# Kernel tuning notes

Measured on AMD Instinct MI355X. Metric: run time of the kernel, lower is better.

## Reference

```python
import jax, jax.numpy as jnp
import numpy as np

N, E, F_IN, H, L, G, C = 50000, 640000, 128, 128, 3, 256, 10
NEG_SLOPE = 0.2  # PyG GATConv default leaky_relu slope


def setup_inputs() -> dict:
    key = jax.random.key(0)
    ks = jax.random.split(key, 10)
    x = jax.random.normal(ks[0], (N, F_IN), jnp.float32)
    edge_index = jax.random.randint(ks[1], (2, E), 0, N, dtype=jnp.int32)
    # sorted graph ids covering all G graphs (global_max_pool segments)
    batch = (jnp.arange(N, dtype=jnp.int32) * G) // N
    s = 1.0 / np.sqrt(H)
    # 3 GAT layers all map 128->128 (F_IN == H), so stack their params
    Wc = jax.random.normal(ks[2], (L, F_IN, H), jnp.float32) * s
    a_src = jax.random.normal(ks[3], (L, H), jnp.float32) * s
    a_dst = jax.random.normal(ks[4], (L, H), jnp.float32) * s
    bc = jnp.zeros((L, H), jnp.float32)
    W1 = jax.random.normal(ks[5], (H, H), jnp.float32) * s
    b1 = jnp.zeros((H,), jnp.float32)
    W2 = jax.random.normal(ks[6], (H, C), jnp.float32) * s
    b2 = jnp.zeros((C,), jnp.float32)
    return dict(x=x, edge_index=edge_index, batch=batch, Wc=Wc, a_src=a_src,
                a_dst=a_dst, bc=bc, W1=W1, b1=b1, W2=W2, b2=b2)


def _gat_layer(h_in, W, a_s, a_d, b, src, dst):
    h = h_in @ W                                   # [N, H]
    e_s = (h * a_s).sum(-1)                        # [N] source term
    e_d = (h * a_d).sum(-1)                        # [N] target term
    e = jax.nn.leaky_relu(e_s[src] + e_d[dst], NEG_SLOPE)  # [E']
    # softmax over incoming edges of each target node
    m = jax.ops.segment_max(e, dst, num_segments=N)
    w = jnp.exp(e - m[dst])
    z = jax.ops.segment_sum(w, dst, num_segments=N)
    alpha = w / (z[dst] + 1e-16)
    out = jax.ops.segment_sum(alpha[:, None] * h[src], dst, num_segments=N)
    return out + b


def reference(x, edge_index, batch, Wc, a_src, a_dst, bc, W1, b1, W2, b2):
    loops = jnp.arange(N, dtype=edge_index.dtype)  # GATConv adds self-loops
    src = jnp.concatenate([edge_index[0], loops])
    dst = jnp.concatenate([edge_index[1], loops])
    h = x
    for l in range(L):
        h = jax.nn.relu(_gat_layer(h, Wc[l], a_src[l], a_dst[l], bc[l], src, dst))
    g = jax.ops.segment_max(h, batch, num_segments=G)  # global_max_pool [G, H]
    g = jax.nn.relu(g @ W1 + b1)
    logits = g @ W2 + b2
    return jax.nn.log_softmax(logits, axis=-1)
```

## Files before the change

### kernel.cpp

```cpp
#include <hip/hip_runtime.h>
#include <hip/hip_fp16.h>
#include <math.h>

#define N_ 50000
#define E_ 640000
#define H_ 128
#define L_ 3
#define G_ 256
#define C_ 10
#define NEG_SLOPE 0.2f

#define ABLK ((N_ + 3) / 4)
#define MAXDEG 64
#define FILL_BLKS 625
#define GEMM_BLKS ((N_ + 63) / 64)

typedef _Float16 half8 __attribute__((ext_vector_type(8)));
typedef float f32x4 __attribute__((ext_vector_type(4)));

__device__ __forceinline__ float leaky(float x) { return x > 0.f ? x : NEG_SLOPE * x; }
__device__ __forceinline__ int pi_out(int p) { return ((p & 7) << 4) + (p >> 3); }

__device__ __forceinline__ void prep_layer(int l, const float* __restrict__ Wc,
                                           const float* __restrict__ a_src,
                                           const float* __restrict__ a_dst,
                                           const float* __restrict__ bc,
                                           __half* __restrict__ Wt,
                                           float* __restrict__ bcp) {
    const float* W = Wc + l * 16384;
    __half* T = Wt + (size_t)l * 144 * 128;
    int t = threadIdx.x;
    for (int e = t; e < 16384; e += 256) {
        int n = e >> 7, p = e & 127;
        int ks = (l == 0) ? p : pi_out(p);
        T[n * 128 + p] = __float2half(W[ks * 128 + n]);
    }
    if (t < 128) {
        int p = t;
        int ks = (l == 0) ? p : pi_out(p);
        const float* as = a_src + l * 128;
        const float* ad = a_dst + l * 128;
        float s = 0.f, d = 0.f;
#pragma unroll 8
        for (int n = 0; n < 128; n++) {
            float w = W[ks * 128 + n];
            s += w * as[n];
            d += w * ad[n];
        }
        T[128 * 128 + p] = __float2half(s);
        T[129 * 128 + p] = __float2half(d);
        bcp[l * 128 + p] = bc[l * 128 + pi_out(p)];
    } else {
        int kk = t - 128;
        for (int r = 130; r < 144; r++) T[r * 128 + kk] = __float2half(0.f);
    }
}

__global__ __launch_bounds__(256) void zero_prep0(int* __restrict__ cur,
                                                  const float* __restrict__ Wc,
                                                  const float* __restrict__ a_src,
                                                  const float* __restrict__ a_dst,
                                                  const float* __restrict__ bc,
                                                  __half* __restrict__ Wt,
                                                  float* __restrict__ bcp) {
    if (blockIdx.x == 0) {
        prep_layer(0, Wc, a_src, a_dst, bc, Wt, bcp);
    } else {
        int i = (blockIdx.x - 1) * 256 + threadIdx.x;
        if (i < N_) cur[i] = 0;
    }
}

template <bool FP16IN>
__device__ __forceinline__ void gemm_body(int bid, const void* __restrict__ Av,
                                          const __half* __restrict__ Wt,
                                          __half* __restrict__ h16,
                                          float* __restrict__ es,
                                          float* __restrict__ ed,
                                          __half* __restrict__ Asw,
                                          __half* __restrict__ Bsw) {
    int tid = threadIdx.x;
    int brow = bid * 64;

    {
        int r = tid >> 2;
        int q = tid & 3;
        int grow = brow + r;
        if (FP16IN) {
            const __half* Ah = (const __half*)Av;
            float4 vv[4];
            if (grow < N_) {
                const float4* p = (const float4*)(Ah + (size_t)grow * 128 + q * 32);
#pragma unroll
                for (int s = 0; s < 4; s++) vv[s] = p[s];
            } else {
                float4 zz = make_float4(0.f, 0.f, 0.f, 0.f);
#pragma unroll
                for (int s = 0; s < 4; s++) vv[s] = zz;
            }
#pragma unroll
            for (int s = 0; s < 4; s++) {
                int kbyte = q * 64 + s * 16;
                int addr = r * 256 + (kbyte ^ ((r & 7) << 4));
                *(float4*)((char*)Asw + addr) = vv[s];
            }
        } else {
            const float* A = (const float*)Av;
            int kc = q * 32;
            float v[32];
            if (grow < N_) {
                const float4* p = (const float4*)(A + (size_t)grow * 128 + kc);
#pragma unroll
                for (int s = 0; s < 8; s++) {
                    float4 f = p[s];
                    v[s * 4] = f.x; v[s * 4 + 1] = f.y; v[s * 4 + 2] = f.z; v[s * 4 + 3] = f.w;
                }
            } else {
#pragma unroll
                for (int s = 0; s < 32; s++) v[s] = 0.f;
            }
#pragma unroll
            for (int s = 0; s < 4; s++) {
                half8 h;
#pragma unroll
                for (int j = 0; j < 8; j++) h[j] = (_Float16)v[s * 8 + j];
                int kbyte = kc * 2 + s * 16;
                int addr = r * 256 + (kbyte ^ ((r & 7) << 4));
                *(half8*)((char*)Asw + addr) = h;
            }
        }
    }
    {
        const float4* src = (const float4*)Wt;
#pragma unroll
        for (int i = 0; i < 9; i++) {
            int c = tid + i * 256;
            int o = c * 16;
            int n = o >> 8;
            float4 val = src[c];
            int addr = n * 256 + ((o & 255) ^ ((n & 7) << 4));
            *(float4*)((char*)Bsw + addr) = val;
        }
    }
    __syncthreads();

    int w = tid >> 6, l = tid & 63;
    int lrow = l & 15, lk = l >> 4;
    f32x4 acc[9];
#pragma unroll
    for (int t = 0; t < 9; t++) acc[t] = (f32x4)0.f;
#pragma unroll
    for (int kk = 0; kk < 4; kk++) {
        int kbyte = kk * 64 + lk * 16;
        int arow = w * 16 + lrow;
        half8 af = *(const half8*)((const char*)Asw + arow * 256 + (kbyte ^ ((arow & 7) << 4)));
#pragma unroll
        for (int t = 0; t < 9; t++) {
            int n = t * 16 + lrow;
            half8 bf = *(const half8*)((const char*)Bsw + n * 256 + (kbyte ^ ((n & 7) << 4)));
            acc[t] = __builtin_amdgcn_mfma_f32_16x16x32_f16(af, bf, acc[t], 0, 0, 0);
        }
    }

    int row0 = brow + w * 16 + lk * 4;
#pragma unroll
    for (int r = 0; r < 4; r++) {
        int grow = row0 + r;
        if (grow < N_) {
            half8 hv;
#pragma unroll
            for (int t = 0; t < 8; t++) hv[t] = (_Float16)acc[t][r];
            *(half8*)(h16 + (size_t)grow * 128 + lrow * 8) = hv;
            if (lrow == 0) es[grow] = acc[8][r];
            else if (lrow == 1) ed[grow] = acc[8][r];
        }
    }
}

__global__ __launch_bounds__(256) void mega0(const int* __restrict__ src,
                                             const int* __restrict__ dst,
                                             int* __restrict__ cur,
                                             int* __restrict__ col_slots,
                                             const float* __restrict__ x,
                                             const float* __restrict__ Wc,
                                             const float* __restrict__ a_src,
                                             const float* __restrict__ a_dst,
                                             const float* __restrict__ bc,
                                             __half* __restrict__ Wt,
                                             float* __restrict__ bcp,
                                             __half* __restrict__ h16,
                                             float* __restrict__ es,
                                             float* __restrict__ ed) {
    __shared__ __half Asw[64 * 128];
    __shared__ __half Bsw[144 * 128];
    int bx = blockIdx.x;
    if (bx < FILL_BLKS) {
        int b = bx * 1024 + threadIdx.x;
        int e0 = b, e1 = b + 256, e2 = b + 512, e3 = b + 768;
        int d0 = dst[e0], d1 = dst[e1], d2 = dst[e2], d3 = dst[e3];
        int s0 = src[e0], s1 = src[e1], s2 = src[e2], s3 = src[e3];
        int p0 = atomicAdd(&cur[d0], 1);
        int p1 = atomicAdd(&cur[d1], 1);
        int p2 = atomicAdd(&cur[d2], 1);
        int p3 = atomicAdd(&cur[d3], 1);
        if (p0 < MAXDEG) col_slots[d0 * MAXDEG + p0] = s0;
        if (p1 < MAXDEG) col_slots[d1 * MAXDEG + p1] = s1;
        if (p2 < MAXDEG) col_slots[d2 * MAXDEG + p2] = s2;
        if (p3 < MAXDEG) col_slots[d3 * MAXDEG + p3] = s3;
    } else if (bx < FILL_BLKS + GEMM_BLKS) {
        gemm_body<false>(bx - FILL_BLKS, x, Wt, h16, es, ed, Asw, Bsw);
    } else {
        prep_layer(bx - (FILL_BLKS + GEMM_BLKS) + 1, Wc, a_src, a_dst, bc, Wt, bcp);
    }
}

template <bool FP16IN>
__global__ __launch_bounds__(256) void gemm_mfma(const void* __restrict__ Av,
                                                 const __half* __restrict__ Wt,
                                                 __half* __restrict__ h16,
                                                 float* __restrict__ es,
                                                 float* __restrict__ ed) {
    __shared__ __half Asw[64 * 128];
    __shared__ __half Bsw[144 * 128];
    gemm_body<FP16IN>(blockIdx.x, Av, Wt, h16, es, ed, Asw, Bsw);
}

__global__ __launch_bounds__(256) void gat_aggregate(const __half* __restrict__ h16,
                                                     const float* __restrict__ es,
                                                     const float* __restrict__ ed,
                                                     const int* __restrict__ cur,
                                                     const int* __restrict__ col_slots,
                                                     const float* __restrict__ biasp,
                                                     __half* __restrict__ hout) {
    __shared__ int   lds_s[4][64];
    __shared__ float lds_w[4][64];
    int wv = threadIdx.x >> 6;
    int lane = threadIdx.x & 63;
    int node = blockIdx.x * 4 + wv;
    if (node >= N_) return;
    int deg = min(cur[node], MAXDEG);
    float edn = ed[node];
    float es_self = es[node];

    int c0 = 0;
    float w0 = 0.f;
    if (lane < deg) {
        c0 = col_slots[node * MAXDEG + lane];
        w0 = __expf(fminf(leaky(es[c0] + edn), 30.f));
    }
    float zl = w0;
    lds_s[wv][lane] = c0;
    lds_w[wv][lane] = w0;

    int eg = lane >> 4;
    int fl = lane & 15;

    float acc[8] = {0.f, 0.f, 0.f, 0.f, 0.f, 0.f, 0.f, 0.f};
#pragma unroll 4
    for (int j = eg; j < deg; j += 4) {
        int s = lds_s[wv][j];
        float a = lds_w[wv][j];
        union { float4 f4; __half2 h2[4]; } u;
        u.f4 = *(const float4*)(h16 + (size_t)s * 128 + fl * 8);
#pragma unroll
        for (int q = 0; q < 4; q++) {
            float2 fv = __half22float2(u.h2[q]);
            acc[2 * q]     += a * fv.x;
            acc[2 * q + 1] += a * fv.y;
        }
    }

#pragma unroll
    for (int q = 0; q < 8; q++) {
        acc[q] += __shfl_xor(acc[q], 16);
        acc[q] += __shfl_xor(acc[q], 32);
    }
#pragma unroll
    for (int o = 32; o; o >>= 1) zl += __shfl_xor(zl, o);
    float ws = __expf(fminf(leaky(es_self + edn), 30.f));
    float inv = 1.0f / (zl + ws + 1e-16f);

    if (eg == 0) {
        union { float4 f4; __half2 h2[4]; } su;
        su.f4 = *(const float4*)(h16 + (size_t)node * 128 + fl * 8);
        const float4* bp = (const float4*)(biasp + fl * 8);
        float4 b0 = bp[0], b1 = bp[1];
        float bq[8] = {b0.x, b0.y, b0.z, b0.w, b1.x, b1.y, b1.z, b1.w};
        union { float4 f4; __half2 h2[4]; } ou;
#pragma unroll
        for (int q = 0; q < 4; q++) {
            float2 sv = __half22float2(su.h2[q]);
            float v0 = fmaxf((acc[2 * q]     + ws * sv.x) * inv + bq[2 * q],     0.f);
            float v1 = fmaxf((acc[2 * q + 1] + ws * sv.y) * inv + bq[2 * q + 1], 0.f);
            ou.h2[q] = __floats2half2_rn(v0, v1);
        }
        *(float4*)(hout + (size_t)node * 128 + fl * 8) = ou.f4;
    }
}

__device__ __forceinline__ int lower_bound_batch(const int* __restrict__ batch, int val) {
    int lo = 0, hi = N_;
    while (lo < hi) {
        int mid = (lo + hi) >> 1;
        if (batch[mid] < val) lo = mid + 1;
        else hi = mid;
    }
    return lo;
}

__global__ __launch_bounds__(512) void pool_head(const __half* __restrict__ h16,
                                                 const int* __restrict__ batch,
                                                 const float* __restrict__ W1,
                                                 const float* __restrict__ b1,
                                                 const float* __restrict__ W2,
                                                 const float* __restrict__ b2,
                                                 float* __restrict__ out) {
    int g = blockIdx.x;
    int t = threadIdx.x;
    __shared__ float red[8][128];
    __shared__ float gs[128], gp[128], lg[C_], lse;

    int s = lower_bound_batch(batch, g);
    int e = lower_bound_batch(batch, g + 1);
    int fs = t & 15;
    int rg = t >> 4;
    float m[8] = {0.f, 0.f, 0.f, 0.f, 0.f, 0.f, 0.f, 0.f};
    for (int i = s + rg; i < e; i += 32) {
        union { float4 f4; __half2 h2[4]; } u;
        u.f4 = *(const float4*)(h16 + (size_t)i * 128 + fs * 8);
#pragma unroll
        for (int q = 0; q < 4; q++) {
            float2 fv = __half22float2(u.h2[q]);
            m[2 * q]     = fmaxf(m[2 * q],     fv.x);
            m[2 * q + 1] = fmaxf(m[2 * q + 1], fv.y);
        }
    }
#pragma unroll
    for (int q = 0; q < 8; q++) {
        m[q] = fmaxf(m[q], __shfl_xor(m[q], 16));
        m[q] = fmaxf(m[q], __shfl_xor(m[q], 32));
    }
    int wid = t >> 6;
    if ((t & 48) == 0) {
#pragma unroll
        for (int q = 0; q < 8; q++) red[wid][fs * 8 + q] = m[q];
    }
    __syncthreads();
    if (t < 128) {
        float mm = red[0][t];
#pragma unroll
        for (int w = 1; w < 8; w++) mm = fmaxf(mm, red[w][t]);
        gs[t] = mm;
    }
    __syncthreads();

    if (t < 128) {
        float acc = b1[t];
#pragma unroll 8
        for (int k = 0; k < 128; k++) {
            int f = pi_out(k);
            acc += gs[k] * W1[f * 128 + t];
        }
        gp[t] = fmaxf(acc, 0.f);
    }
    __syncthreads();
    if (t < C_) {
        float a2 = b2[t];
#pragma unroll 8
        for (int k = 0; k < 128; k++) a2 += gp[k] * W2[k * C_ + t];
        lg[t] = a2;
    }
    __syncthreads();
    if (t == 0) {
        float mm = lg[0];
#pragma unroll
        for (int i = 1; i < C_; i++) mm = fmaxf(mm, lg[i]);
        float ss = 0.f;
#pragma unroll
        for (int i = 0; i < C_; i++) ss += expf(lg[i] - mm);
        lse = mm + logf(ss);
    }
    __syncthreads();
    if (t < C_) out[g * C_ + t] = lg[t] - lse;
}

extern "C" void kernel_launch(void* const* d_in, const int* in_sizes, int n_in,
                              void* d_out, int out_size, void* d_ws, size_t ws_size,
                              hipStream_t stream) {
    const float* x     = (const float*)d_in[0];
    const int*   eidx  = (const int*)d_in[1];
    const int*   batch = (const int*)d_in[2];
    const float* Wc    = (const float*)d_in[3];
    const float* a_src = (const float*)d_in[4];
    const float* a_dst = (const float*)d_in[5];
    const float* bc    = (const float*)d_in[6];
    const float* W1    = (const float*)d_in[7];
    const float* b1    = (const float*)d_in[8];
    const float* W2    = (const float*)d_in[9];
    const float* b2    = (const float*)d_in[10];
    float* out = (float*)d_out;

    const int* srcs = eidx;
    const int* dsts = eidx + E_;

    __half* hG16  = (__half*)d_ws;
    __half* hB16  = hG16 + (size_t)N_ * 128;
    float*  es    = (float*)(hB16 + (size_t)N_ * 128);
    float*  ed    = es + N_;
    float*  bcp   = ed + N_;
    __half* Wt    = (__half*)(bcp + 3 * 128);
    int*    cur       = (int*)(Wt + (size_t)3 * 144 * 128);
    int*    col_slots = cur + N_;

    zero_prep0<<<1 + (N_ + 255) / 256, 256, 0, stream>>>(cur, Wc, a_src, a_dst, bc, Wt, bcp);

    mega0<<<FILL_BLKS + GEMM_BLKS + 2, 256, 0, stream>>>(
        srcs, dsts, cur, col_slots, x, Wc, a_src, a_dst, bc, Wt, bcp, hG16, es, ed);

    gat_aggregate<<<ABLK, 256, 0, stream>>>(hG16, es, ed, cur, col_slots, bcp, hB16);
    for (int l = 1; l < L_; ++l) {
        gemm_mfma<true><<<GEMM_BLKS, 256, 0, stream>>>(
            hB16, Wt + (size_t)l * 144 * 128, hG16, es, ed);
        gat_aggregate<<<ABLK, 256, 0, stream>>>(hG16, es, ed, cur, col_slots,
                                                bcp + l * 128, hB16);
    }

    pool_head<<<G_, 512, 0, stream>>>(hB16, batch, W1, b1, W2, b2, out);
}
```

Before: 203.6 us.

## Fuse CSR slot fill into layer-0 GEMM blocks and prep all layers upfront

Instead of a heterogeneous mega kernel with separate fill blocks and GEMM blocks, every GEMM block now also handles four edges per thread. It issues the edge index loads and atomics early so their latency overlaps the x load, LDS staging and MFMA work, then writes col_slots at the end. Weight prep for all three layers moves into the zeroing kernel. The aggregate kernel now loads col_slots unconditionally, clamping the value, so the load is not serialized behind the degree read. This may read uninitialized slots, which is harmless because of the clamp, and it adds atomic traffic to the GEMM blocks.

```diff
diff --git a/kernel.cpp b/kernel.cpp
--- a/kernel.cpp
+++ b/kernel.cpp
@@ -12,8 +12,8 @@
 
 #define ABLK ((N_ + 3) / 4)
 #define MAXDEG 64
-#define FILL_BLKS 625
 #define GEMM_BLKS ((N_ + 63) / 64)
+#define FILL_T (GEMM_BLKS * 256)
 
 typedef _Float16 half8 __attribute__((ext_vector_type(8)));
 typedef float f32x4 __attribute__((ext_vector_type(4)));
@@ -56,88 +56,80 @@
     }
 }
 
-__global__ __launch_bounds__(256) void zero_prep0(int* __restrict__ cur,
-                                                  const float* __restrict__ Wc,
-                                                  const float* __restrict__ a_src,
-                                                  const float* __restrict__ a_dst,
-                                                  const float* __restrict__ bc,
-                                                  __half* __restrict__ Wt,
-                                                  float* __restrict__ bcp) {
-    if (blockIdx.x == 0) {
-        prep_layer(0, Wc, a_src, a_dst, bc, Wt, bcp);
+__global__ __launch_bounds__(256) void zero_prep(int* __restrict__ cur,
+                                                 const float* __restrict__ Wc,
+                                                 const float* __restrict__ a_src,
+                                                 const float* __restrict__ a_dst,
+                                                 const float* __restrict__ bc,
+                                                 __half* __restrict__ Wt,
+                                                 float* __restrict__ bcp) {
+    if (blockIdx.x < L_) {
+        prep_layer(blockIdx.x, Wc, a_src, a_dst, bc, Wt, bcp);
     } else {
-        int i = (blockIdx.x - 1) * 256 + threadIdx.x;
+        int i = (blockIdx.x - L_) * 256 + threadIdx.x;
         if (i < N_) cur[i] = 0;
     }
 }
 
-template <bool FP16IN>
-__device__ __forceinline__ void gemm_body(int bid, const void* __restrict__ Av,
-                                          const __half* __restrict__ Wt,
-                                          __half* __restrict__ h16,
-                                          float* __restrict__ es,
-                                          float* __restrict__ ed,
-                                          __half* __restrict__ Asw,
-                                          __half* __restrict__ Bsw) {
+__global__ __launch_bounds__(256) void gemm0_fill(const float* __restrict__ A,
+                                                  const __half* __restrict__ Wt,
+                                                  __half* __restrict__ h16,
+                                                  float* __restrict__ es,
+                                                  float* __restrict__ ed,
+                                                  const int* __restrict__ src,
+                                                  const int* __restrict__ dst,
+                                                  int* __restrict__ cur,
+                                                  int* __restrict__ col_slots) {
+    __shared__ __half Asw[64 * 128];
+    __shared__ __half Bsw[144 * 128];
     int tid = threadIdx.x;
-    int brow = bid * 64;
-
+    int brow = blockIdx.x * 64;
+
+    int g = blockIdx.x * 256 + tid;
+    int e1 = g + FILL_T, e2 = g + 2 * FILL_T, e3 = g + 3 * FILL_T;
+    bool v3 = e3 < E_;
+    int d0 = dst[g], d1 = dst[e1], d2 = dst[e2];
+    int s0 = src[g], s1 = src[e1], s2 = src[e2];
+    int d3 = 0, s3 = 0;
+    if (v3) { d3 = dst[e3]; s3 = src[e3]; }
+
+    int r = tid >> 2, q = tid & 3, kc = q * 32, grow = brow + r;
+    float v[32];
+    if (grow < N_) {
+        const float4* p = (const float4*)(A + (size_t)grow * 128 + kc);
+#pragma unroll
+        for (int s = 0; s < 8; s++) {
+            float4 f = p[s];
+            v[s * 4] = f.x; v[s * 4 + 1] = f.y; v[s * 4 + 2] = f.z; v[s * 4 + 3] = f.w;
+        }
+    } else {
+#pragma unroll
+        for (int s = 0; s < 32; s++) v[s] = 0.f;
+    }
+
+    int p0 = atomicAdd(&cur[d0], 1);
+    int p1 = atomicAdd(&cur[d1], 1);
+    int p2 = atomicAdd(&cur[d2], 1);
+    int p3 = MAXDEG;
+    if (v3) p3 = atomicAdd(&cur[d3], 1);
+
+#pragma unroll
+    for (int s = 0; s < 4; s++) {
+        half8 h;
+#pragma unroll
+        for (int j = 0; j < 8; j++) h[j] = (_Float16)v[s * 8 + j];
+        int kbyte = kc * 2 + s * 16;
+        int addr = r * 256 + (kbyte ^ ((r & 7) << 4));
+        *(half8*)((char*)Asw + addr) = h;
+    }
     {
-        int r = tid >> 2;
-        int q = tid & 3;
-        int grow = brow + r;
-        if (FP16IN) {
-            const __half* Ah = (const __half*)Av;
-            float4 vv[4];
-            if (grow < N_) {
-                const float4* p = (const float4*)(Ah + (size_t)grow * 128 + q * 32);
-#pragma unroll
-                for (int s = 0; s < 4; s++) vv[s] = p[s];
-            } else {
-                float4 zz = make_float4(0.f, 0.f, 0.f, 0.f);
-#pragma unroll
-                for (int s = 0; s < 4; s++) vv[s] = zz;
-            }
-#pragma unroll
-            for (int s = 0; s < 4; s++) {
-                int kbyte = q * 64 + s * 16;
-                int addr = r * 256 + (kbyte ^ ((r & 7) << 4));
-                *(float4*)((char*)Asw + addr) = vv[s];
-            }
-        } else {
-            const float* A = (const float*)Av;
-            int kc = q * 32;
-            float v[32];
-            if (grow < N_) {
-                const float4* p = (const float4*)(A + (size_t)grow * 128 + kc);
-#pragma unroll
-                for (int s = 0; s < 8; s++) {
-                    float4 f = p[s];
-                    v[s * 4] = f.x; v[s * 4 + 1] = f.y; v[s * 4 + 2] = f.z; v[s * 4 + 3] = f.w;
-                }
-            } else {
-#pragma unroll
-                for (int s = 0; s < 32; s++) v[s] = 0.f;
-            }
-#pragma unroll
-            for (int s = 0; s < 4; s++) {
-                half8 h;
-#pragma unroll
-                for (int j = 0; j < 8; j++) h[j] = (_Float16)v[s * 8 + j];
-                int kbyte = kc * 2 + s * 16;
-                int addr = r * 256 + (kbyte ^ ((r & 7) << 4));
-                *(half8*)((char*)Asw + addr) = h;
-            }
-        }
-    }
-    {
-        const float4* src = (const float4*)Wt;
+        const float4* srcW = (const float4*)Wt;
 #pragma unroll
         for (int i = 0; i < 9; i++) {
             int c = tid + i * 256;
             int o = c * 16;
             int n = o >> 8;
-            float4 val = src[c];
+            float4 val = srcW[c];
             int addr = n * 256 + ((o & 255) ^ ((n & 7) << 4));
             *(float4*)((char*)Bsw + addr) = val;
         }
@@ -164,65 +156,98 @@
 
     int row0 = brow + w * 16 + lk * 4;
 #pragma unroll
-    for (int r = 0; r < 4; r++) {
-        int grow = row0 + r;
-        if (grow < N_) {
+    for (int rr = 0; rr < 4; rr++) {
+        int gr = row0 + rr;
+        if (gr < N_) {
             half8 hv;
 #pragma unroll
-            for (int t = 0; t < 8; t++) hv[t] = (_Float16)acc[t][r];
-            *(half8*)(h16 + (size_t)grow * 128 + lrow * 8) = hv;
-            if (lrow == 0) es[grow] = acc[8][r];
-            else if (lrow == 1) ed[grow] = acc[8][r];
-        }
-    }
-}
-
-__global__ __launch_bounds__(256) void mega0(const int* __restrict__ src,
-                                             const int* __restrict__ dst,
-                                             int* __restrict__ cur,
-                                             int* __restrict__ col_slots,
-                                             const float* __restrict__ x,
-                                             const float* __restrict__ Wc,
-                                             const float* __restrict__ a_src,
-                                             const float* __restrict__ a_dst,
-                                             const float* __restrict__ bc,
-                                             __half* __restrict__ Wt,
-                                             float* __restrict__ bcp,
-                                             __half* __restrict__ h16,
-                                             float* __restrict__ es,
-                                             float* __restrict__ ed) {
-    __shared__ __half Asw[64 * 128];
-    __shared__ __half Bsw[144 * 128];
-    int bx = blockIdx.x;
-    if (bx < FILL_BLKS) {
-        int b = bx * 1024 + threadIdx.x;
-        int e0 = b, e1 = b + 256, e2 = b + 512, e3 = b + 768;
-        int d0 = dst[e0], d1 = dst[e1], d2 = dst[e2], d3 = dst[e3];
-        int s0 = src[e0], s1 = src[e1], s2 = src[e2], s3 = src[e3];
-        int p0 = atomicAdd(&cur[d0], 1);
-        int p1 = atomicAdd(&cur[d1], 1);
-        int p2 = atomicAdd(&cur[d2], 1);
-        int p3 = atomicAdd(&cur[d3], 1);
-        if (p0 < MAXDEG) col_slots[d0 * MAXDEG + p0] = s0;
-        if (p1 < MAXDEG) col_slots[d1 * MAXDEG + p1] = s1;
-        if (p2 < MAXDEG) col_slots[d2 * MAXDEG + p2] = s2;
-        if (p3 < MAXDEG) col_slots[d3 * MAXDEG + p3] = s3;
-    } else if (bx < FILL_BLKS + GEMM_BLKS) {
-        gemm_body<false>(bx - FILL_BLKS, x, Wt, h16, es, ed, Asw, Bsw);
-    } else {
-        prep_layer(bx - (FILL_BLKS + GEMM_BLKS) + 1, Wc, a_src, a_dst, bc, Wt, bcp);
-    }
-}
-
-template <bool FP16IN>
-__global__ __launch_bounds__(256) void gemm_mfma(const void* __restrict__ Av,
+            for (int t = 0; t < 8; t++) hv[t] = (_Float16)acc[t][rr];
+            *(half8*)(h16 + (size_t)gr * 128 + lrow * 8) = hv;
+            if (lrow == 0) es[gr] = acc[8][rr];
+            else if (lrow == 1) ed[gr] = acc[8][rr];
+        }
+    }
+
+    if (p0 < MAXDEG) col_slots[d0 * MAXDEG + p0] = s0;
+    if (p1 < MAXDEG) col_slots[d1 * MAXDEG + p1] = s1;
+    if (p2 < MAXDEG) col_slots[d2 * MAXDEG + p2] = s2;
+    if (p3 < MAXDEG) col_slots[d3 * MAXDEG + p3] = s3;
+}
+
+__global__ __launch_bounds__(256) void gemm_mfma(const __half* __restrict__ Ah,
                                                  const __half* __restrict__ Wt,
                                                  __half* __restrict__ h16,
                                                  float* __restrict__ es,
                                                  float* __restrict__ ed) {
     __shared__ __half Asw[64 * 128];
     __shared__ __half Bsw[144 * 128];
-    gemm_body<FP16IN>(blockIdx.x, Av, Wt, h16, es, ed, Asw, Bsw);
+    int tid = threadIdx.x;
+    int brow = blockIdx.x * 64;
+
+    {
+        int r = tid >> 2, q = tid & 3, grow = brow + r;
+        float4 vv[4];
+        if (grow < N_) {
+            const float4* p = (const float4*)(Ah + (size_t)grow * 128 + q * 32);
+#pragma unroll
+            for (int s = 0; s < 4; s++) vv[s] = p[s];
+        } else {
+            float4 zz = make_float4(0.f, 0.f, 0.f, 0.f);
+#pragma unroll
+            for (int s = 0; s < 4; s++) vv[s] = zz;
+        }
+#pragma unroll
+        for (int s = 0; s < 4; s++) {
+            int kbyte = q * 64 + s * 16;
+            int addr = r * 256 + (kbyte ^ ((r & 7) << 4));
+            *(float4*)((char*)Asw + addr) = vv[s];
+        }
+    }
+    {
+        const float4* srcW = (const float4*)Wt;
+#pragma unroll
+        for (int i = 0; i < 9; i++) {
+            int c = tid + i * 256;
+            int o = c * 16;
+            int n = o >> 8;
+            float4 val = srcW[c];
+            int addr = n * 256 + ((o & 255) ^ ((n & 7) << 4));
+            *(float4*)((char*)Bsw + addr) = val;
+        }
+    }
+    __syncthreads();
+
+    int w = tid >> 6, l = tid & 63;
+    int lrow = l & 15, lk = l >> 4;
+    f32x4 acc[9];
+#pragma unroll
+    for (int t = 0; t < 9; t++) acc[t] = (f32x4)0.f;
+#pragma unroll
+    for (int kk = 0; kk < 4; kk++) {
+        int kbyte = kk * 64 + lk * 16;
+        int arow = w * 16 + lrow;
+        half8 af = *(const half8*)((const char*)Asw + arow * 256 + (kbyte ^ ((arow & 7) << 4)));
+#pragma unroll
+        for (int t = 0; t < 9; t++) {
+            int n = t * 16 + lrow;
+            half8 bf = *(const half8*)((const char*)Bsw + n * 256 + (kbyte ^ ((n & 7) << 4)));
+            acc[t] = __builtin_amdgcn_mfma_f32_16x16x32_f16(af, bf, acc[t], 0, 0, 0);
+        }
+    }
+
+    int row0 = brow + w * 16 + lk * 4;
+#pragma unroll
+    for (int rr = 0; rr < 4; rr++) {
+        int gr = row0 + rr;
+        if (gr < N_) {
+            half8 hv;
+#pragma unroll
+            for (int t = 0; t < 8; t++) hv[t] = (_Float16)acc[t][rr];
+            *(half8*)(h16 + (size_t)gr * 128 + lrow * 8) = hv;
+            if (lrow == 0) es[gr] = acc[8][rr];
+            else if (lrow == 1) ed[gr] = acc[8][rr];
+        }
+    }
 }
 
 __global__ __launch_bounds__(256) void gat_aggregate(const __half* __restrict__ h16,
@@ -238,18 +263,19 @@
     int lane = threadIdx.x & 63;
     int node = blockIdx.x * 4 + wv;
     if (node >= N_) return;
-    int deg = min(cur[node], MAXDEG);
+
+    int deg_raw = cur[node];
+    int craw = col_slots[node * MAXDEG + lane];
     float edn = ed[node];
     float es_self = es[node];
 
-    int c0 = 0;
+    int deg = min(deg_raw, MAXDEG);
+    int c0 = min(max(craw, 0), N_ - 1);
+    lds_s[wv][lane] = c0;
+
     float w0 = 0.f;
-    if (lane < deg) {
-        c0 = col_slots[node * MAXDEG + lane];
-        w0 = __expf(fminf(leaky(es[c0] + edn), 30.f));
-    }
+    if (lane < deg) w0 = __expf(fminf(leaky(es[c0] + edn), 30.f));
     float zl = w0;
-    lds_s[wv][lane] = c0;
     lds_w[wv][lane] = w0;
 
     int eg = lane >> 4;
@@ -263,17 +289,17 @@
         union { float4 f4; __half2 h2[4]; } u;
         u.f4 = *(const float4*)(h16 + (size_t)s * 128 + fl * 8);
 #pragma unroll
-        for (int q = 0; q < 4; q++) {
-            float2 fv = __half22float2(u.h2[q]);
-            acc[2 * q]     += a * fv.x;
-            acc[2 * q + 1] += a * fv.y;
-        }
-    }
-
-#pragma unroll
-    for (int q = 0; q < 8; q++) {
-        acc[q] += __shfl_xor(acc[q], 16);
-        acc[q] += __shfl_xor(acc[q], 32);
+        for (int qq = 0; qq < 4; qq++) {
+            float2 fv = __half22float2(u.h2[qq]);
+            acc[2 * qq]     += a * fv.x;
+            acc[2 * qq + 1] += a * fv.y;
+        }
+    }
+
+#pragma unroll
+    for (int qq = 0; qq < 8; qq++) {
+        acc[qq] += __shfl_xor(acc[qq], 16);
+        acc[qq] += __shfl_xor(acc[qq], 32);
     }
 #pragma unroll
     for (int o = 32; o; o >>= 1) zl += __shfl_xor(zl, o);
@@ -288,11 +314,11 @@
         float bq[8] = {b0.x, b0.y, b0.z, b0.w, b1.x, b1.y, b1.z, b1.w};
         union { float4 f4; __half2 h2[4]; } ou;
 #pragma unroll
-        for (int q = 0; q < 4; q++) {
-            float2 sv = __half22float2(su.h2[q]);
-            float v0 = fmaxf((acc[2 * q]     + ws * sv.x) * inv + bq[2 * q],     0.f);
-            float v1 = fmaxf((acc[2 * q + 1] + ws * sv.y) * inv + bq[2 * q + 1], 0.f);
-            ou.h2[q] = __floats2half2_rn(v0, v1);
+        for (int qq = 0; qq < 4; qq++) {
+            float2 sv = __half22float2(su.h2[qq]);
+            float v0 = fmaxf((acc[2 * qq]     + ws * sv.x) * inv + bq[2 * qq],     0.f);
+            float v1 = fmaxf((acc[2 * qq + 1] + ws * sv.y) * inv + bq[2 * qq + 1], 0.f);
+            ou.h2[qq] = __floats2half2_rn(v0, v1);
         }
         *(float4*)(hout + (size_t)node * 128 + fl * 8) = ou.f4;
     }
@@ -329,21 +355,21 @@
         union { float4 f4; __half2 h2[4]; } u;
         u.f4 = *(const float4*)(h16 + (size_t)i * 128 + fs * 8);
 #pragma unroll
-        for (int q = 0; q < 4; q++) {
-            float2 fv = __half22float2(u.h2[q]);
-            m[2 * q]     = fmaxf(m[2 * q],     fv.x);
-            m[2 * q + 1] = fmaxf(m[2 * q + 1], fv.y);
-        }
-    }
-#pragma unroll
-    for (int q = 0; q < 8; q++) {
-        m[q] = fmaxf(m[q], __shfl_xor(m[q], 16));
-        m[q] = fmaxf(m[q], __shfl_xor(m[q], 32));
+        for (int qq = 0; qq < 4; qq++) {
+            float2 fv = __half22float2(u.h2[qq]);
+            m[2 * qq]     = fmaxf(m[2 * qq],     fv.x);
+            m[2 * qq + 1] = fmaxf(m[2 * qq + 1], fv.y);
+        }
+    }
+#pragma unroll
+    for (int qq = 0; qq < 8; qq++) {
+        m[qq] = fmaxf(m[qq], __shfl_xor(m[qq], 16));
+        m[qq] = fmaxf(m[qq], __shfl_xor(m[qq], 32));
     }
     int wid = t >> 6;
     if ((t & 48) == 0) {
 #pragma unroll
-        for (int q = 0; q < 8; q++) red[wid][fs * 8 + q] = m[q];
+        for (int qq = 0; qq < 8; qq++) red[wid][fs * 8 + qq] = m[qq];
     }
     __syncthreads();
     if (t < 128) {
@@ -412,14 +438,14 @@
     int*    cur       = (int*)(Wt + (size_t)3 * 144 * 128);
     int*    col_slots = cur + N_;
 
-    zero_prep0<<<1 + (N_ + 255) / 256, 256, 0, stream>>>(cur, Wc, a_src, a_dst, bc, Wt, bcp);
-
-    mega0<<<FILL_BLKS + GEMM_BLKS + 2, 256, 0, stream>>>(
-        srcs, dsts, cur, col_slots, x, Wc, a_src, a_dst, bc, Wt, bcp, hG16, es, ed);
+    zero_prep<<<L_ + (N_ + 255) / 256, 256, 0, stream>>>(cur, Wc, a_src, a_dst, bc, Wt, bcp);
+
+    gemm0_fill<<<GEMM_BLKS, 256, 0, stream>>>(x, Wt, hG16, es, ed,
+                                              srcs, dsts, cur, col_slots);
 
     gat_aggregate<<<ABLK, 256, 0, stream>>>(hG16, es, ed, cur, col_slots, bcp, hB16);
     for (int l = 1; l < L_; ++l) {
-        gemm_mfma<true><<<GEMM_BLKS, 256, 0, stream>>>(
+        gemm_mfma<<<GEMM_BLKS, 256, 0, stream>>>(
             hB16, Wt + (size_t)l * 144 * 128, hG16, es, ed);
         gat_aggregate<<<ABLK, 256, 0, stream>>>(hG16, es, ed, cur, col_slots,
                                                 bcp + l * 128, hB16);
```

Result: faster. 188.4 us (-7.4%).
